# Optimization experiments

Hardware: AMD Instinct MI355X
Metric: run time of the kernel (lower is better)

The kernel has to match this reference:

```python
import jax, jax.numpy as jnp
import numpy as np
from jax.scipy.special import logsumexp

B, S, H, L = 64, 512, 768, 9  # batch, seq_len, bert hidden, num CoNLL labels


def setup_inputs() -> dict:
    key = jax.random.key(0)
    ks = jax.random.split(key, 7)
    hidden = jax.random.normal(ks[0], (B, S, H), jnp.float32)
    cls_w = jax.random.normal(ks[1], (H, L), jnp.float32) * 0.02
    cls_b = jnp.zeros((L,), jnp.float32)
    # pytorch-crf initializes params uniform(-0.1, 0.1)
    start_transitions = jax.random.uniform(ks[2], (L,), jnp.float32, -0.1, 0.1)
    end_transitions = jax.random.uniform(ks[3], (L,), jnp.float32, -0.1, 0.1)
    transitions = jax.random.uniform(ks[4], (L, L), jnp.float32, -0.1, 0.1)
    labels = jax.random.randint(ks[5], (B, S), 0, L).astype(jnp.int64)
    attention_mask = jnp.ones((B, S), jnp.int32)  # CRF requires mask[:, 0] True
    return dict(hidden=hidden, cls_w=cls_w, cls_b=cls_b,
                start_transitions=start_transitions,
                end_transitions=end_transitions, transitions=transitions,
                labels=labels, attention_mask=attention_mask)


def _crf_nll(emissions, tags, mask, start_transitions, end_transitions, transitions):
    # emissions [B,S,L], tags [B,S] int, mask [B,S] bool. pytorch-crf, batch_first.
    maskf = mask.astype(emissions.dtype)
    b = emissions.shape[0]
    # ---- numerator: score of the given tag path ----
    em_tag = jnp.take_along_axis(emissions, tags[..., None], axis=2)[..., 0]  # [B,S]
    trans_score = transitions[tags[:, :-1], tags[:, 1:]]                      # [B,S-1]
    num = (start_transitions[tags[:, 0]] + em_tag[:, 0]
           + jnp.sum((trans_score + em_tag[:, 1:]) * maskf[:, 1:], axis=1))
    seq_ends = jnp.sum(mask, axis=1).astype(jnp.int32) - 1
    last_tags = jnp.take_along_axis(tags, seq_ends[:, None].astype(tags.dtype), axis=1)[:, 0]
    num = num + end_transitions[last_tags]
    # ---- denominator: forward algorithm (log partition) as a scan ----
    def step(score, xs):
        em_t, m_t = xs  # [B,L], [B]
        nxt = logsumexp(score[:, :, None] + transitions[None] + em_t[:, None, :], axis=1)
        return jnp.where(m_t[:, None], nxt, score), None

    init = start_transitions[None, :] + emissions[:, 0]  # [B,L]
    xs = (jnp.swapaxes(emissions[:, 1:], 0, 1), jnp.swapaxes(mask[:, 1:], 0, 1))
    final, _ = jax.lax.scan(step, init, xs)
    denom = logsumexp(final + end_transitions[None, :], axis=1)  # [B]
    llh = num - denom
    return -jnp.mean(llh)  # reduction='mean' over batch, then negated


def reference(hidden, cls_w, cls_b, start_transitions, end_transitions,
              transitions, labels, attention_mask):
    # dropout in eval mode -> identity
    emissions = hidden @ cls_w + cls_b  # [B,S,L]
    mask = attention_mask.astype(bool)
    tags = jnp.where(labels == -100, 0, labels)  # clamp ignored labels to 0
    loss = _crf_nll(emissions, tags, mask, start_transitions,
                    end_transitions, transitions)
    return (loss, emissions)
```

## Files before the change

kernel.cpp:

```cpp
#include <hip/hip_runtime.h>
#include <cstdint>

#define BB 64
#define SS 512
#define HH 768
#define LL 9
#define NROWS (BB * SS)
#define NCHUNK 16
#define CLEN 32

#define L2E 1.4426950408889634f
#define LN2 0.6931471805599453f
#define NEGINF (-1e30f)

typedef __attribute__((ext_vector_type(8))) short bf16x8;
typedef __attribute__((ext_vector_type(4))) float f32x4;

__device__ inline short f2bf(float f) {
  uint32_t u = __builtin_bit_cast(uint32_t, f);
  return (short)((u + 0x8000u) >> 16);
}

__global__ __launch_bounds__(256) void pack_w(const float* __restrict__ w,
                                              uint4* __restrict__ wfrag) {
  const int e = blockIdx.x * 256 + threadIdx.x;
  if (e >= 24 * 64) return;
  const int c = e >> 6, l = e & 63;
  const int col = l & 15, g = l >> 4;
  const int k0 = c * 32 + g * 8;
  uint32_t pk[4];
#pragma unroll
  for (int p = 0; p < 4; ++p) {
    const float lo = (col < LL) ? w[(k0 + 2 * p) * LL + col] : 0.f;
    const float hi = (col < LL) ? w[(k0 + 2 * p + 1) * LL + col] : 0.f;
    pk[p] = (uint32_t)(uint16_t)f2bf(lo) | ((uint32_t)(uint16_t)f2bf(hi) << 16);
  }
  wfrag[e] = make_uint4(pk[0], pk[1], pk[2], pk[3]);
}

__global__ __launch_bounds__(256) void emis_gemm(
    const float* __restrict__ hidden, const uint4* __restrict__ wfrag,
    const float* __restrict__ bias, float* __restrict__ emis) {
  const int lane = threadIdx.x & 63;
  const int wv = threadIdx.x >> 6;
  const int m0 = (blockIdx.x * 4 + wv) * 16;
  const int g = lane >> 4;
  const int row = m0 + (lane & 15);
  const float4* __restrict__ hp =
      reinterpret_cast<const float4*>(hidden + (size_t)row * HH) + 2 * g;
  const bf16x8* __restrict__ bf = reinterpret_cast<const bf16x8*>(wfrag);

  f32x4 acc = {0.f, 0.f, 0.f, 0.f};
#pragma unroll 4
  for (int kt = 0; kt < 24; ++kt) {
    const float4 h0 = hp[kt * 8];
    const float4 h1 = hp[kt * 8 + 1];
    union { short s[8]; bf16x8 v; } a;
    a.s[0] = f2bf(h0.x); a.s[1] = f2bf(h0.y); a.s[2] = f2bf(h0.z); a.s[3] = f2bf(h0.w);
    a.s[4] = f2bf(h1.x); a.s[5] = f2bf(h1.y); a.s[6] = f2bf(h1.z); a.s[7] = f2bf(h1.w);
    const bf16x8 b = bf[kt * 64 + lane];
    acc = __builtin_amdgcn_mfma_f32_16x16x32_bf16(a.v, b, acc, 0, 0, 0);
  }
  const int col = lane & 15;
  if (col < LL) {
    const float bcol = bias[col];
#pragma unroll
    for (int r = 0; r < 4; ++r) {
      const int rr = m0 + g * 4 + r;
      emis[(size_t)rr * LL + col] = acc[r] + bcol;
    }
  }
}

__global__ __launch_bounds__(128) void crf_chunk(
    const float* __restrict__ emis, const int* __restrict__ msk,
    const float* __restrict__ startT, const float* __restrict__ trans,
    float* __restrict__ initv, float* __restrict__ Pmat) {
  __shared__ float em_lds[CLEN * LL];
  __shared__ int mk_lds[CLEN];
  const int b = blockIdx.x >> 4;
  const int c = blockIdx.x & 15;
  const int tid = threadIdx.x;
  const int lane = tid & 63;
  const int wid = tid >> 6;

  const float* src = emis + ((size_t)b * SS + c * CLEN) * LL;
  for (int i = tid; i < CLEN * LL; i += 128) em_lds[i] = src[i];
  for (int i = tid; i < CLEN; i += 128) mk_lds[i] = msk[b * SS + c * CLEN + i];
  __syncthreads();

  int rloc = lane / 9;
  int j = lane - rloc * 9;
  if (rloc > 6) { rloc = 6; j = 8; }
  const int rbase = rloc * 9;
  const bool active = (wid == 0) ? (lane < 63) : (lane < 18);
  const int r = wid * 7 + rloc;

  float Tc[LL];
#pragma unroll
  for (int i = 0; i < LL; ++i) Tc[i] = trans[i * LL + j];

  float s;
  if (c == 0) s = startT[j] + em_lds[j];
  else s = (j == r) ? 0.f : NEGINF;
  const int t0 = (c == 0) ? 1 : 0;

  for (int t = t0; t < CLEN; ++t) {
    const float emj = em_lds[t * LL + j];
    const int mt = mk_lds[t];
    const float s0 = __shfl(s, rbase + 0), s1 = __shfl(s, rbase + 1), s2 = __shfl(s, rbase + 2);
    const float s3 = __shfl(s, rbase + 3), s4 = __shfl(s, rbase + 4), s5 = __shfl(s, rbase + 5);
    const float s6 = __shfl(s, rbase + 6), s7 = __shfl(s, rbase + 7), s8 = __shfl(s, rbase + 8);
    const float a0 = s0 + Tc[0], a1 = s1 + Tc[1], a2 = s2 + Tc[2];
    const float a3 = s3 + Tc[3], a4 = s4 + Tc[4], a5 = s5 + Tc[5];
    const float a6 = s6 + Tc[6], a7 = s7 + Tc[7], a8 = s8 + Tc[8];
    const float m = fmaxf(fmaxf(fmaxf(fmaxf(a0, a1), fmaxf(a2, a3)),
                                fmaxf(fmaxf(a4, a5), fmaxf(a6, a7))), a8);
    const float e =
        ((exp2f((a0 - m) * L2E) + exp2f((a1 - m) * L2E)) +
         (exp2f((a2 - m) * L2E) + exp2f((a3 - m) * L2E))) +
        ((exp2f((a4 - m) * L2E) + exp2f((a5 - m) * L2E)) +
         (exp2f((a6 - m) * L2E) + exp2f((a7 - m) * L2E))) +
        exp2f((a8 - m) * L2E);
    const float snew = m + LN2 * log2f(e) + emj;
    s = mt ? snew : s;
  }

  if (active) {
    if (c == 0) {
      if (wid == 0 && lane < LL) initv[b * LL + j] = s;
    } else {
      Pmat[((size_t)b * NCHUNK + c) * 81 + r * LL + j] = s;
    }
  }
}

__global__ __launch_bounds__(64) void crf_combine(
    const float* __restrict__ emis, const int* __restrict__ labels,
    const int* __restrict__ msk, const float* __restrict__ startT,
    const float* __restrict__ endT, const float* __restrict__ trans,
    const float* __restrict__ initv, const float* __restrict__ Pmat,
    float* __restrict__ llh) {
  __shared__ float Pl[15 * 81];
  const int b = blockIdx.x;
  const int lane = threadIdx.x;
  const float* __restrict__ emb = emis + (size_t)b * SS * LL;
  const int* __restrict__ lab = labels + b * SS;
  const int* __restrict__ mk = msk + b * SS;

  const float* Pb = Pmat + (size_t)b * NCHUNK * 81 + 81;
  for (int i = lane; i < 15 * 81; i += 64) Pl[i] = Pb[i];

  float acc = 0.f;
  int msum = 0;
  for (int t = lane; t < SS; t += 64) {
    int tg = lab[t]; if (tg == -100) tg = 0;
    const int mt = mk[t];
    msum += mt;
    if (t == 0) {
      acc += startT[tg] + emb[tg];
    } else {
      int tp = lab[t - 1]; if (tp == -100) tp = 0;
      acc += (trans[tp * LL + tg] + emb[t * LL + tg]) * (float)mt;
    }
  }
#pragma unroll
  for (int off = 32; off; off >>= 1) {
    acc += __shfl_xor(acc, off);
    msum += __shfl_xor(msum, off);
  }
  const int seq_end = msum - 1;
  int lt = lab[seq_end]; if (lt == -100) lt = 0;
  const float num = acc + endT[lt];

  __syncthreads();

  const int j = (lane < LL) ? lane : 8;
  float a = initv[b * LL + j];
#pragma unroll 1
  for (int c = 0; c < 15; ++c) {
    const float* P = &Pl[c * 81];
    const float s0 = __shfl(a, 0), s1 = __shfl(a, 1), s2 = __shfl(a, 2);
    const float s3 = __shfl(a, 3), s4 = __shfl(a, 4), s5 = __shfl(a, 5);
    const float s6 = __shfl(a, 6), s7 = __shfl(a, 7), s8 = __shfl(a, 8);
    const float a0 = s0 + P[0 * LL + j], a1 = s1 + P[1 * LL + j], a2 = s2 + P[2 * LL + j];
    const float a3 = s3 + P[3 * LL + j], a4 = s4 + P[4 * LL + j], a5 = s5 + P[5 * LL + j];
    const float a6 = s6 + P[6 * LL + j], a7 = s7 + P[7 * LL + j], a8 = s8 + P[8 * LL + j];
    const float m = fmaxf(fmaxf(fmaxf(fmaxf(a0, a1), fmaxf(a2, a3)),
                                fmaxf(fmaxf(a4, a5), fmaxf(a6, a7))), a8);
    const float e =
        ((exp2f((a0 - m) * L2E) + exp2f((a1 - m) * L2E)) +
         (exp2f((a2 - m) * L2E) + exp2f((a3 - m) * L2E))) +
        ((exp2f((a4 - m) * L2E) + exp2f((a5 - m) * L2E)) +
         (exp2f((a6 - m) * L2E) + exp2f((a7 - m) * L2E))) +
        exp2f((a8 - m) * L2E);
    a = m + LN2 * log2f(e);
  }
  a += endT[j];
  {
    const float s0 = __shfl(a, 0), s1 = __shfl(a, 1), s2 = __shfl(a, 2);
    const float s3 = __shfl(a, 3), s4 = __shfl(a, 4), s5 = __shfl(a, 5);
    const float s6 = __shfl(a, 6), s7 = __shfl(a, 7), s8 = __shfl(a, 8);
    const float m = fmaxf(fmaxf(fmaxf(fmaxf(s0, s1), fmaxf(s2, s3)),
                                fmaxf(fmaxf(s4, s5), fmaxf(s6, s7))), s8);
    const float e =
        ((exp2f((s0 - m) * L2E) + exp2f((s1 - m) * L2E)) +
         (exp2f((s2 - m) * L2E) + exp2f((s3 - m) * L2E))) +
        ((exp2f((s4 - m) * L2E) + exp2f((s5 - m) * L2E)) +
         (exp2f((s6 - m) * L2E) + exp2f((s7 - m) * L2E))) +
        exp2f((s8 - m) * L2E);
    const float denom = m + LN2 * log2f(e);
    if (lane == 0) llh[b] = num - denom;
  }
}

__global__ __launch_bounds__(64) void finalize(const float* __restrict__ llh,
                                               float* __restrict__ out) {
  float v = llh[threadIdx.x];
#pragma unroll
  for (int off = 32; off; off >>= 1) v += __shfl_xor(v, off);
  if (threadIdx.x == 0) out[0] = -v * (1.0f / BB);
}

extern "C" void kernel_launch(void* const* d_in, const int* in_sizes, int n_in,
                              void* d_out, int out_size, void* d_ws, size_t ws_size,
                              hipStream_t stream) {
  const float* hidden = (const float*)d_in[0];
  const float* cls_w  = (const float*)d_in[1];
  const float* cls_b  = (const float*)d_in[2];
  const float* startT = (const float*)d_in[3];
  const float* endT   = (const float*)d_in[4];
  const float* trans  = (const float*)d_in[5];
  const int* labels   = (const int*)d_in[6];
  const int* amask    = (const int*)d_in[7];

  float* out = (float*)d_out;
  float* emis = out + 1;

  float* llh = (float*)d_ws;
  float* initv = llh + 64;
  float* Pmat = initv + 64 * LL;
  uint4* wfrag = (uint4*)(Pmat + (size_t)BB * NCHUNK * 81);

  pack_w<<<6, 256, 0, stream>>>(cls_w, wfrag);
  emis_gemm<<<NROWS / 64, 256, 0, stream>>>(hidden, wfrag, cls_b, emis);
  crf_chunk<<<BB * NCHUNK, 128, 0, stream>>>(emis, amask, startT, trans, initv, Pmat);
  crf_combine<<<BB, 64, 0, stream>>>(emis, labels, amask, startT, endT, trans, initv, Pmat, llh);
  finalize<<<1, 64, 0, stream>>>(llh, out);
}
```

Before: 198.6 us.

## Stage hidden rows through swizzled LDS with coalesced loads and register-resident weights

The emission GEMM now loads hidden rows cooperatively with fully coalesced float4 reads, converts them to bf16 and stores them into an XOR-swizzled LDS tile. Each wave then reads its MFMA A-fragments from LDS. All 24 weight fragments are preloaded into registers, and the next global chunk is prefetched while the MFMAs run. This targets the strided per-lane global access pattern of the old direct-load loop, at the cost of LDS traffic, two barriers per stage and higher register pressure (launch bounds set to 2 blocks).

After: 206.2 us. 1.04x slower.

```diff
diff --git a/kernel.cpp b/kernel.cpp
--- a/kernel.cpp
+++ b/kernel.cpp
@@ -16,9 +16,12 @@
 typedef __attribute__((ext_vector_type(8))) short bf16x8;
 typedef __attribute__((ext_vector_type(4))) float f32x4;
 
-__device__ inline short f2bf(float f) {
+__device__ inline uint32_t f2bf_u(float f) {
   uint32_t u = __builtin_bit_cast(uint32_t, f);
-  return (short)((u + 0x8000u) >> 16);
+  return (u + 0x8000u) >> 16;
+}
+__device__ inline uint32_t pack2(float a, float b) {
+  return f2bf_u(a) | (f2bf_u(b) << 16);
 }
 
 __global__ __launch_bounds__(256) void pack_w(const float* __restrict__ w,
@@ -33,40 +36,72 @@
   for (int p = 0; p < 4; ++p) {
     const float lo = (col < LL) ? w[(k0 + 2 * p) * LL + col] : 0.f;
     const float hi = (col < LL) ? w[(k0 + 2 * p + 1) * LL + col] : 0.f;
-    pk[p] = (uint32_t)(uint16_t)f2bf(lo) | ((uint32_t)(uint16_t)f2bf(hi) << 16);
+    pk[p] = pack2(lo, hi);
   }
   wfrag[e] = make_uint4(pk[0], pk[1], pk[2], pk[3]);
 }
 
-__global__ __launch_bounds__(256) void emis_gemm(
+__global__ __launch_bounds__(256, 2) void emis_gemm(
     const float* __restrict__ hidden, const uint4* __restrict__ wfrag,
     const float* __restrict__ bias, float* __restrict__ emis) {
-  const int lane = threadIdx.x & 63;
-  const int wv = threadIdx.x >> 6;
-  const int m0 = (blockIdx.x * 4 + wv) * 16;
+  __shared__ uint4 lds4[64 * 16];
+  unsigned char* lds = reinterpret_cast<unsigned char*>(lds4);
+  const int tid = threadIdx.x;
+  const int lane = tid & 63;
+  const int wv = tid >> 6;
+  const int m0 = blockIdx.x * 64;
+
+  bf16x8 Wf[24];
+  const bf16x8* __restrict__ bf = reinterpret_cast<const bf16x8*>(wfrag);
+#pragma unroll
+  for (int kt = 0; kt < 24; ++kt) Wf[kt] = bf[kt * 64 + lane];
+
+  const int srow = tid >> 2;
+  const int sq = tid & 3;
+  const float4* __restrict__ gsrc =
+      reinterpret_cast<const float4*>(hidden + (size_t)(m0 + srow) * HH);
+  const int swz = (srow & 7) << 4;
+  unsigned char* wbase = lds + srow * 256;
+
+  const int crow = lane & 15;
   const int g = lane >> 4;
-  const int row = m0 + (lane & 15);
-  const float4* __restrict__ hp =
-      reinterpret_cast<const float4*>(hidden + (size_t)row * HH) + 2 * g;
-  const bf16x8* __restrict__ bf = reinterpret_cast<const bf16x8*>(wfrag);
+  const int rswz = (crow & 7) << 4;
+  const unsigned char* rbase = lds + (wv * 16 + crow) * 256;
+
+  float4 h[8];
+#pragma unroll
+  for (int u = 0; u < 8; ++u) h[u] = gsrc[sq + 4 * u];
 
   f32x4 acc = {0.f, 0.f, 0.f, 0.f};
-#pragma unroll 4
-  for (int kt = 0; kt < 24; ++kt) {
-    const float4 h0 = hp[kt * 8];
-    const float4 h1 = hp[kt * 8 + 1];
-    union { short s[8]; bf16x8 v; } a;
-    a.s[0] = f2bf(h0.x); a.s[1] = f2bf(h0.y); a.s[2] = f2bf(h0.z); a.s[3] = f2bf(h0.w);
-    a.s[4] = f2bf(h1.x); a.s[5] = f2bf(h1.y); a.s[6] = f2bf(h1.z); a.s[7] = f2bf(h1.w);
-    const bf16x8 b = bf[kt * 64 + lane];
-    acc = __builtin_amdgcn_mfma_f32_16x16x32_bf16(a.v, b, acc, 0, 0, 0);
-  }
+#pragma unroll
+  for (int s = 0; s < 6; ++s) {
+#pragma unroll
+    for (int u = 0; u < 8; ++u) {
+      const uint32_t lo = pack2(h[u].x, h[u].y);
+      const uint32_t hi = pack2(h[u].z, h[u].w);
+      const int off = (((sq + 4 * u) * 8) ^ swz);
+      *reinterpret_cast<uint2*>(wbase + off) = make_uint2(lo, hi);
+    }
+    __syncthreads();
+    if (s < 5) {
+#pragma unroll
+      for (int u = 0; u < 8; ++u) h[u] = gsrc[(s + 1) * 32 + sq + 4 * u];
+    }
+#pragma unroll
+    for (int ks = 0; ks < 4; ++ks) {
+      const bf16x8 a = *reinterpret_cast<const bf16x8*>(
+          rbase + (((ks * 64 + g * 16) ^ rswz)));
+      acc = __builtin_amdgcn_mfma_f32_16x16x32_bf16(a, Wf[s * 4 + ks], acc, 0, 0, 0);
+    }
+    __syncthreads();
+  }
+
   const int col = lane & 15;
   if (col < LL) {
     const float bcol = bias[col];
 #pragma unroll
     for (int r = 0; r < 4; ++r) {
-      const int rr = m0 + g * 4 + r;
+      const int rr = m0 + wv * 16 + g * 4 + r;
       emis[(size_t)rr * LL + col] = acc[r] + bcol;
     }
   }
```
